# Optimization experiments

Hardware: AMD Instinct MI355X
Metric: run time of the kernel (lower is better)

Reference implementation:

```python
import jax, jax.numpy as jnp
import numpy as np

NH, K = 16, 4  # num_heads, num_points


def _ln(x, g, b):
    m = x.mean(-1, keepdims=True)
    v = jnp.var(x, axis=-1, keepdims=True)
    return (x - m) / jnp.sqrt(v + 1e-5) * g + b


def setup_inputs() -> dict:
    key = jax.random.key(0)
    ks = jax.random.split(key, 12)
    B, S, D = 16, 1024, 1024
    HD = D // NH
    def lin(k, fi, fo, scale=1.0):
        return jax.random.normal(k, (fi, fo), jnp.float32) * (scale / np.sqrt(fi))
    z = lambda n: jnp.zeros((n,), jnp.float32)
    return {
        "source": jax.random.normal(ks[0], (B, S, D), jnp.float32),
        "target": jax.random.normal(ks[1], (B, S, D), jnp.float32),
        "Wq": lin(ks[2], D, D), "bq": z(D),
        "Wo1": lin(ks[3], HD, 64), "bo1": z(64),
        "Wo2": lin(ks[4], 64, 2 * K, 0.1), "bo2": z(2 * K),
        "Wa": lin(ks[5], HD, K), "ba": z(K),
        "Wv": lin(ks[6], D, D), "bv": z(D),
        "Wout": lin(ks[7], D, D), "bout": z(D),
        "gq": jnp.ones((D,), jnp.float32), "bq_ln": z(D),
        "gkv": jnp.ones((D,), jnp.float32), "bkv_ln": z(D),
        "gffn": jnp.ones((D,), jnp.float32), "bffn_ln": z(D),
        "W1": lin(ks[8], D, 4 * D), "b1": z(4 * D),
        "W2": lin(ks[9], 4 * D, D), "b2": z(D),
    }


def _forward(source, target, Wq, bq, Wo1, bo1, Wo2, bo2, Wa, ba, Wv, bv,
             Wout, bout, gq, bq_ln, gkv, bkv_ln, gffn, bffn_ln, W1, b1, W2, b2):
    B, S, D = source.shape
    HD = D // NH
    Hs = int(round(S ** 0.5)); Ws = Hs  # S = H*W square grid

    q_norm = _ln(source, gq, bq_ln)
    v_norm = _ln(target, gkv, bkv_ln)
    q = (q_norm @ Wq + bq).reshape(B, S, NH, HD)
    # value map per head: (B, NH, H, W, HD)
    v = (v_norm @ Wv + bv).reshape(B, Hs, Ws, NH, HD).transpose(0, 3, 1, 2, 4)
    v_flat = v.reshape(B, NH, Hs * Ws, HD)

    # learned offsets: tanh(MLP(q)) * 0.5, in normalized [-1,1] coords
    h = jax.nn.relu(q @ Wo1 + bo1)
    off = jnp.tanh((h @ Wo2 + bo2).reshape(B, S, NH, K, 2)) * 0.5

    # reference grid: ref_grid[i*W+j] = (ref_x[j], ref_y[i])
    rx = jnp.linspace(-1.0, 1.0, Ws)
    ry = jnp.linspace(-1.0, 1.0, Hs)
    gx, gy = jnp.meshgrid(rx, ry)  # 'xy' indexing
    ref = jnp.stack([gx, gy], -1).reshape(S, 2)
    pts = ref[None, :, None, None, :] + off  # (B, S, NH, K, 2), last dim = (x, y)

    # grid_sample, bilinear, align_corners=True, padding_mode='zeros'
    x = (pts[..., 0] + 1.0) * 0.5 * (Ws - 1)
    y = (pts[..., 1] + 1.0) * 0.5 * (Hs - 1)
    x = jnp.moveaxis(x, 1, 2)  # (B, NH, S, K)
    y = jnp.moveaxis(y, 1, 2)
    x0 = jnp.floor(x); y0 = jnp.floor(y)
    wx1 = x - x0; wy1 = y - y0
    x0i = x0.astype(jnp.int32); y0i = y0.astype(jnp.int32)

    def gather(xi, yi, w):
        m = (xi >= 0) & (xi <= Ws - 1) & (yi >= 0) & (yi <= Hs - 1)
        idx = jnp.clip(yi, 0, Hs - 1) * Ws + jnp.clip(xi, 0, Ws - 1)
        g = jnp.take_along_axis(v_flat, idx.reshape(B, NH, S * K, 1), axis=2)
        return g.reshape(B, NH, S, K, HD) * (w * m)[..., None]

    sampled = (gather(x0i, y0i, (1.0 - wx1) * (1.0 - wy1))
               + gather(x0i + 1, y0i, wx1 * (1.0 - wy1))
               + gather(x0i, y0i + 1, (1.0 - wx1) * wy1)
               + gather(x0i + 1, y0i + 1, wx1 * wy1))  # (B, NH, S, K, HD)

    attn = jax.nn.softmax(q @ Wa + ba, axis=-1)  # (B, S, NH, K)
    head_out = jnp.einsum('bsnk,bnskd->bsnd', attn, sampled).reshape(B, S, D)

    src = source + (head_out @ Wout + bout)
    f = jax.nn.gelu(_ln(src, gffn, bffn_ln) @ W1 + b1, approximate=False)
    return src + (f @ W2 + b2)


def reference(source, target, Wq, bq, Wo1, bo1, Wo2, bo2, Wa, ba, Wv, bv,
              Wout, bout, gq, bq_ln, gkv, bkv_ln, gffn, bffn_ln, W1, b1, W2, b2):
    return _forward(source, target, Wq, bq, Wo1, bo1, Wo2, bo2, Wa, ba, Wv, bv,
                    Wout, bout, gq, bq_ln, gkv, bkv_ln, gffn, bffn_ln, W1, b1, W2, b2)
```

## Files before the change

### kernel.cpp

```cpp
#include <hip/hip_runtime.h>

typedef __attribute__((ext_vector_type(8))) short short8;
typedef __attribute__((ext_vector_type(16))) float f32x16;

#define DEV __device__ __forceinline__

DEV float bf2f(unsigned short u) { return __uint_as_float(((unsigned)u) << 16); }
DEV unsigned short f2bf(float f) {
  unsigned u = __float_as_uint(f);
  u += 0x7FFF + ((u >> 16) & 1);
  return (unsigned short)(u >> 16);
}

#define GLOAD_LDS16(gptr, lptr)                                                              \
  __builtin_amdgcn_global_load_lds((const __attribute__((address_space(1))) void*)(gptr),   \
                                   (__attribute__((address_space(3))) void*)(lptr), 16, 0, 0)

__global__ __launch_bounds__(256) void wt_transpose_bf16(const float* __restrict__ W,
                                                         unsigned short* __restrict__ Wt,
                                                         int K, int N) {
  __shared__ float t[32][33];
  int k0 = blockIdx.x * 32, n0 = blockIdx.y * 32;
  int tx = threadIdx.x, ty = threadIdx.y;
#pragma unroll
  for (int i = 0; i < 4; ++i)
    t[ty + 8 * i][tx] = W[(long)(k0 + ty + 8 * i) * N + n0 + tx];
  __syncthreads();
#pragma unroll
  for (int i = 0; i < 4; ++i)
    Wt[(long)(n0 + ty + 8 * i) * K + k0 + tx] = f2bf(t[tx][ty + 8 * i]);
}

__global__ __launch_bounds__(256) void ln_to_bf16_dual(
    const float* __restrict__ x0, const float* __restrict__ g0, const float* __restrict__ b0,
    unsigned short* __restrict__ y0,
    const float* __restrict__ x1, const float* __restrict__ g1, const float* __restrict__ b1,
    unsigned short* __restrict__ y1) {
  const bool second = blockIdx.x >= 16384;
  const long row = second ? blockIdx.x - 16384 : blockIdx.x;
  const float* x = second ? x1 : x0;
  const float* g = second ? g1 : g0;
  const float* b = second ? b1 : b0;
  unsigned short* y = second ? y1 : y0;
  const int tid = threadIdx.x;
  float4 v = *(const float4*)(x + row * 1024 + tid * 4);
  float s = v.x + v.y + v.z + v.w;
  float s2 = v.x * v.x + v.y * v.y + v.z * v.z + v.w * v.w;
#pragma unroll
  for (int o = 32; o > 0; o >>= 1) { s += __shfl_down(s, o); s2 += __shfl_down(s2, o); }
  __shared__ float red[8];
  __shared__ float mv[2];
  int wv = tid >> 6, ln = tid & 63;
  if (ln == 0) { red[wv] = s; red[4 + wv] = s2; }
  __syncthreads();
  if (tid == 0) {
    float a = red[0] + red[1] + red[2] + red[3];
    float q = red[4] + red[5] + red[6] + red[7];
    float mean = a * (1.f / 1024.f);
    mv[0] = mean;
    mv[1] = rsqrtf(q * (1.f / 1024.f) - mean * mean + 1e-5f);
  }
  __syncthreads();
  float mean = mv[0], rstd = mv[1];
  float4 gg = *(const float4*)(g + tid * 4);
  float4 bb = *(const float4*)(b + tid * 4);
  ushort4 o;
  o.x = f2bf((v.x - mean) * rstd * gg.x + bb.x);
  o.y = f2bf((v.y - mean) * rstd * gg.y + bb.y);
  o.z = f2bf((v.z - mean) * rstd * gg.z + bb.z);
  o.w = f2bf((v.w - mean) * rstd * gg.w + bb.w);
  *(ushort4*)(y + row * 1024 + tid * 4) = o;
}

__global__ __launch_bounds__(256) void ln_to_bf16(const float* __restrict__ x,
                                                  const float* __restrict__ g,
                                                  const float* __restrict__ b,
                                                  unsigned short* __restrict__ y) {
  const long row = blockIdx.x;
  const int tid = threadIdx.x;
  float4 v = *(const float4*)(x + row * 1024 + tid * 4);
  float s = v.x + v.y + v.z + v.w;
  float s2 = v.x * v.x + v.y * v.y + v.z * v.z + v.w * v.w;
#pragma unroll
  for (int o = 32; o > 0; o >>= 1) { s += __shfl_down(s, o); s2 += __shfl_down(s2, o); }
  __shared__ float red[8];
  __shared__ float mv[2];
  int wv = tid >> 6, ln = tid & 63;
  if (ln == 0) { red[wv] = s; red[4 + wv] = s2; }
  __syncthreads();
  if (tid == 0) {
    float a = red[0] + red[1] + red[2] + red[3];
    float q = red[4] + red[5] + red[6] + red[7];
    float mean = a * (1.f / 1024.f);
    mv[0] = mean;
    mv[1] = rsqrtf(q * (1.f / 1024.f) - mean * mean + 1e-5f);
  }
  __syncthreads();
  float mean = mv[0], rstd = mv[1];
  float4 gg = *(const float4*)(g + tid * 4);
  float4 bb = *(const float4*)(b + tid * 4);
  ushort4 o;
  o.x = f2bf((v.x - mean) * rstd * gg.x + bb.x);
  o.y = f2bf((v.y - mean) * rstd * gg.y + bb.y);
  o.z = f2bf((v.z - mean) * rstd * gg.z + bb.z);
  o.w = f2bf((v.w - mean) * rstd * gg.w + bb.w);
  *(ushort4*)(y + row * 1024 + tid * 4) = o;
}

template <int EPI>
DEV void epi_store(void* out, const float* res, long grow, long gcol, int N, float val) {
  if (EPI == 0) {
    ((unsigned short*)out)[grow * N + gcol] = f2bf(val);
  } else if (EPI == 1) {
    const int b_ = (int)(grow >> 10), hw = (int)(grow & 1023);
    const int nh = (int)(gcol >> 6), hd = (int)(gcol & 63);
    ((unsigned short*)out)[((long)(b_ * 16 + nh) << 16) + hw * 64 + hd] = f2bf(val);
  } else if (EPI == 2) {
    ((float*)out)[grow * N + gcol] = val + res[grow * N + gcol];
  } else if (EPI == 3) {
    const float c = 0.79788456080286536f;
    float t = tanhf(c * (val + 0.044715f * val * val * val));
    ((unsigned short*)out)[grow * N + gcol] = f2bf(0.5f * val * (1.f + t));
  } else {
    ((float*)out)[grow * N + gcol] = val + res[grow * N + gcol];
  }
}

template <int EPI>
__global__ __launch_bounds__(256, 4) void gemm32(const unsigned short* __restrict__ A,
                                                 const unsigned short* __restrict__ Bt,
                                                 const float* __restrict__ bias,
                                                 const float* __restrict__ res,
                                                 void* __restrict__ out,
                                                 int N, int K, int ldb, int n_mt) {
  __shared__ __align__(16) char smem[32768];
  const int tid = threadIdx.x;
  const int wave = tid >> 6, lane = tid & 63;
  const int wm = wave >> 1, wn = wave & 1;

  const int st = blockIdx.x >> 5, wi = blockIdx.x & 31;
  const int nsm = n_mt >> 3;
  const int stm = st % nsm, stn = st / nsm;
  const long row0 = (long)(stm * 8 + (wi & 7)) * 128;
  const long col0 = (long)(stn * 4 + (wi >> 3)) * 128;

  f32x16 acc[2][2];
#pragma unroll
  for (int i = 0; i < 2; ++i)
#pragma unroll
    for (int n = 0; n < 2; ++n)
#pragma unroll
      for (int r = 0; r < 16; ++r) acc[i][n][r] = 0.f;

  const int rin = lane >> 3, ch = lane & 7;

  for (int kt = 0; kt < K; kt += 64) {
#pragma unroll
    for (int i = 0; i < 4; ++i) {
      const int c = wave * 4 + i;
      const int r = c * 8 + rin;
      const int kg = ch ^ ((r >> 1) & 7);
      GLOAD_LDS16(A + (row0 + r) * (long)K + kt + kg * 8, smem + c * 1024);
      GLOAD_LDS16(Bt + (col0 + r) * (long)ldb + kt + kg * 8, smem + 16384 + c * 1024);
    }
    asm volatile("s_waitcnt vmcnt(0)" ::: "memory");
    __syncthreads();
#pragma unroll
    for (int ks = 0; ks < 4; ++ks) {
      short8 af[2], bfr[2];
      const int kc = ks * 2 + (lane >> 5);
#pragma unroll
      for (int mi = 0; mi < 2; ++mi) {
        const int rowa = wm * 64 + mi * 32 + (lane & 31);
        af[mi] = *(const short8*)(smem + rowa * 128 + (kc ^ ((rowa >> 1) & 7)) * 16);
      }
#pragma unroll
      for (int ni = 0; ni < 2; ++ni) {
        const int rowb = wn * 64 + ni * 32 + (lane & 31);
        bfr[ni] = *(const short8*)(smem + 16384 + rowb * 128 + (kc ^ ((rowb >> 1) & 7)) * 16);
      }
#pragma unroll
      for (int mi = 0; mi < 2; ++mi)
#pragma unroll
        for (int ni = 0; ni < 2; ++ni)
          acc[mi][ni] =
              __builtin_amdgcn_mfma_f32_32x32x16_bf16(af[mi], bfr[ni], acc[mi][ni], 0, 0, 0);
    }
    __syncthreads();
  }

  const int lc = lane & 31, lh = lane >> 5;
#pragma unroll
  for (int mi = 0; mi < 2; ++mi)
#pragma unroll
    for (int ni = 0; ni < 2; ++ni) {
      const long gcol = col0 + wn * 64 + ni * 32 + lc;
      const float bvv = (EPI == 5) ? 0.f : bias[gcol];
#pragma unroll
      for (int reg = 0; reg < 16; ++reg) {
        const long grow = row0 + wm * 64 + mi * 32 + (reg & 3) + 8 * (reg >> 2) + 4 * lh;
        epi_store<EPI>(out, res, grow, gcol, N, acc[mi][ni][reg] + bvv);
      }
    }
}

__global__ __launch_bounds__(256) void offset_attn_mlp(
    const unsigned short* __restrict__ qf,
    const float* __restrict__ Wo1, const float* __restrict__ bo1,
    const float* __restrict__ Wo2, const float* __restrict__ bo2,
    const float* __restrict__ Wa, const float* __restrict__ ba,
    float* __restrict__ coords) {
  const int r = blockIdx.x * 256 + threadIdx.x;
  const int s = (r >> 4) & 1023;

  float qr[64];
  const unsigned short* qp = qf + (long)r * 64;
#pragma unroll
  for (int i = 0; i < 8; ++i) {
    short8 v = *(const short8*)(qp + 8 * i);
#pragma unroll
    for (int j = 0; j < 8; ++j) qr[8 * i + j] = bf2f((unsigned short)v[j]);
  }

  float off[8];
#pragma unroll
  for (int o = 0; o < 8; ++o) off[o] = bo2[o];

#pragma unroll 1
  for (int jj = 0; jj < 8; ++jj) {
    float hacc[8];
#pragma unroll
    for (int o = 0; o < 8; ++o) hacc[o] = bo1[jj * 8 + o];
#pragma unroll
    for (int i = 0; i < 64; ++i) {
      const float qv = qr[i];
#pragma unroll
      for (int o = 0; o < 8; ++o) hacc[o] = fmaf(qv, Wo1[i * 64 + jj * 8 + o], hacc[o]);
    }
#pragma unroll
    for (int jo = 0; jo < 8; ++jo) {
      const float hj = fmaxf(hacc[jo], 0.f);
      const int j = jj * 8 + jo;
#pragma unroll
      for (int o = 0; o < 8; ++o) off[o] = fmaf(hj, Wo2[j * 8 + o], off[o]);
    }
  }

  float lg[4];
#pragma unroll
  for (int k = 0; k < 4; ++k) lg[k] = ba[k];
#pragma unroll
  for (int i = 0; i < 64; ++i) {
    const float qv = qr[i];
#pragma unroll
    for (int k = 0; k < 4; ++k) lg[k] = fmaf(qv, Wa[i * 4 + k], lg[k]);
  }
  const float mx = fmaxf(fmaxf(lg[0], lg[1]), fmaxf(lg[2], lg[3]));
  const float e0 = expf(lg[0] - mx), e1 = expf(lg[1] - mx), e2 = expf(lg[2] - mx),
              e3 = expf(lg[3] - mx);
  const float inv = 1.f / (e0 + e1 + e2 + e3);

  const float sx = (float)(s & 31), sy = (float)(s >> 5);
  float4 xv, yv, av;
  xv.x = sx + tanhf(off[0]) * 7.75f; yv.x = sy + tanhf(off[1]) * 7.75f;
  xv.y = sx + tanhf(off[2]) * 7.75f; yv.y = sy + tanhf(off[3]) * 7.75f;
  xv.z = sx + tanhf(off[4]) * 7.75f; yv.z = sy + tanhf(off[5]) * 7.75f;
  xv.w = sx + tanhf(off[6]) * 7.75f; yv.w = sy + tanhf(off[7]) * 7.75f;
  av.x = e0 * inv; av.y = e1 * inv; av.z = e2 * inv; av.w = e3 * inv;
  float* cp = coords + (long)r * 16;
  *(float4*)(cp + 0) = xv;
  *(float4*)(cp + 4) = yv;
  *(float4*)(cp + 8) = av;
}

__global__ __launch_bounds__(256) void deform_gather(
    const unsigned short* __restrict__ v_flat, const float* __restrict__ coords,
    unsigned short* __restrict__ head_out) {
  const int tid = threadIdx.x, wave = tid >> 6, lane = tid & 63;
  const int m = blockIdx.x * 4 + wave;
  const int b = m >> 14, nh = (m >> 10) & 15, s = m & 1023;
  const long r = (long)(b * 1024 + s) * 16 + nh;

  float cf = 0.f;
  if (lane < 12) cf = coords[r * 16 + lane];
  const unsigned short* vb = v_flat + ((long)(b * 16 + nh) << 16);

  float o = 0.f;
#pragma unroll
  for (int k = 0; k < 4; ++k) {
    const float xp = __shfl(cf, k), yp = __shfl(cf, 4 + k), ak = __shfl(cf, 8 + k);
    const float x0f = floorf(xp), y0f = floorf(yp);
    const int x0 = (int)x0f, y0 = (int)y0f;
    const float wx1 = xp - x0f, wy1 = yp - y0f;
    const float wx0 = 1.f - wx1, wy0 = 1.f - wy1;
    float smp = 0.f;
#pragma unroll
    for (int cn = 0; cn < 4; ++cn) {
      const int xi = x0 + (cn & 1), yi = y0 + (cn >> 1);
      const float w = (cn & 1 ? wx1 : wx0) * (cn >> 1 ? wy1 : wy0);
      const bool msk = (xi >= 0) & (xi <= 31) & (yi >= 0) & (yi <= 31);
      const int xc = min(max(xi, 0), 31), yc = min(max(yi, 0), 31);
      const float vv = bf2f(vb[(yc * 32 + xc) * 64 + lane]);
      smp = fmaf(vv, msk ? w : 0.f, smp);
    }
    o = fmaf(ak, smp, o);
  }
  head_out[r * 64 + lane] = f2bf(o);
}

extern "C" void kernel_launch(void* const* d_in, const int* in_sizes, int n_in,
                              void* d_out, int out_size, void* d_ws, size_t ws_size,
                              hipStream_t stream) {
  const float* source = (const float*)d_in[0];
  const float* target = (const float*)d_in[1];
  const float* Wq = (const float*)d_in[2];
  const float* bq = (const float*)d_in[3];
  const float* Wo1 = (const float*)d_in[4];
  const float* bo1 = (const float*)d_in[5];
  const float* Wo2 = (const float*)d_in[6];
  const float* bo2 = (const float*)d_in[7];
  const float* Wa = (const float*)d_in[8];
  const float* ba = (const float*)d_in[9];
  const float* Wv = (const float*)d_in[10];
  const float* bv = (const float*)d_in[11];
  const float* Wout = (const float*)d_in[12];
  const float* bout = (const float*)d_in[13];
  const float* gq = (const float*)d_in[14];
  const float* bq_ln = (const float*)d_in[15];
  const float* gkv = (const float*)d_in[16];
  const float* bkv_ln = (const float*)d_in[17];
  const float* gffn = (const float*)d_in[18];
  const float* bffn_ln = (const float*)d_in[19];
  const float* W1 = (const float*)d_in[20];
  const float* b1 = (const float*)d_in[21];
  const float* W2 = (const float*)d_in[22];
  const float* b2 = (const float*)d_in[23];

  char* ws = (char*)d_ws;
  const size_t MB = 1u << 20;
  if (ws_size < 150 * MB) return;
  const bool big = (ws_size >= 182 * MB);

  unsigned short* q_norm = (unsigned short*)(ws + 0);
  unsigned short* v_flat = (unsigned short*)(ws + 0);
  unsigned short* v_norm = (unsigned short*)(ws + 32 * MB);
  float* coords = (float*)(ws + 32 * MB);
  unsigned short* qf = (unsigned short*)(ws + 64 * MB);
  unsigned short* head_out = (unsigned short*)(ws + 96 * MB);
  unsigned short* ffn_in = (unsigned short*)(big ? ws + 128 * MB : ws + 32 * MB);
  unsigned short* f_buf = (unsigned short*)(big ? ws + 0 : ws + 64 * MB);
  char* wbase = big ? ws + 160 * MB : ws + 128 * MB;
  unsigned short* Wq_t = (unsigned short*)(wbase + 0);
  unsigned short* Wv_t = (unsigned short*)(wbase + 2 * MB);
  unsigned short* Wout_t = (unsigned short*)(wbase + 4 * MB);
  unsigned short* W1_t = (unsigned short*)(wbase + 6 * MB);
  unsigned short* W2_t = (unsigned short*)(wbase + 14 * MB);
  float* src = (float*)d_out;

  dim3 tb(32, 8);
  wt_transpose_bf16<<<dim3(32, 32), tb, 0, stream>>>(Wq, Wq_t, 1024, 1024);
  wt_transpose_bf16<<<dim3(32, 32), tb, 0, stream>>>(Wv, Wv_t, 1024, 1024);
  wt_transpose_bf16<<<dim3(32, 32), tb, 0, stream>>>(Wout, Wout_t, 1024, 1024);
  wt_transpose_bf16<<<dim3(32, 128), tb, 0, stream>>>(W1, W1_t, 1024, 4096);
  wt_transpose_bf16<<<dim3(128, 32), tb, 0, stream>>>(W2, W2_t, 4096, 1024);

  ln_to_bf16_dual<<<32768, 256, 0, stream>>>(source, gq, bq_ln, q_norm,
                                             target, gkv, bkv_ln, v_norm);

  gemm32<0><<<1024, 256, 0, stream>>>(q_norm, Wq_t, bq, nullptr, qf, 1024, 1024, 1024, 128);
  gemm32<1><<<1024, 256, 0, stream>>>(v_norm, Wv_t, bv, nullptr, v_flat, 1024, 1024, 1024, 128);

  offset_attn_mlp<<<1024, 256, 0, stream>>>(qf, Wo1, bo1, Wo2, bo2, Wa, ba, coords);
  deform_gather<<<65536, 256, 0, stream>>>(v_flat, coords, head_out);

  gemm32<2><<<1024, 256, 0, stream>>>(head_out, Wout_t, bout, source, src, 1024, 1024, 1024, 128);

  ln_to_bf16<<<16384, 256, 0, stream>>>(src, gffn, bffn_ln, ffn_in);

  if (big) {
    gemm32<3><<<4096, 256, 0, stream>>>(ffn_in, W1_t, b1, nullptr, f_buf, 4096, 1024, 1024, 128);
    gemm32<2><<<1024, 256, 0, stream>>>(f_buf, W2_t, b2, src, src, 1024, 4096, 4096, 128);
  } else {
    gemm32<3><<<2048, 256, 0, stream>>>(ffn_in, W1_t, b1, nullptr, f_buf, 2048, 1024, 1024, 128);
    gemm32<2><<<1024, 256, 0, stream>>>(f_buf, W2_t, b2, src, src, 1024, 2048, 4096, 128);
    gemm32<3><<<2048, 256, 0, stream>>>(ffn_in, W1_t + (long)2048 * 1024, b1 + 2048,
                                        nullptr, f_buf, 2048, 1024, 1024, 128);
    gemm32<5><<<1024, 256, 0, stream>>>(f_buf, W2_t + 2048, nullptr, src, src, 1024, 2048, 4096, 128);
  }
}
```

Measured before the change: 702.2 us.

## Use warp-specialized producer/consumer GEMM for the FFN up-projection

Adds a gemm_pc kernel with 512 threads per block. Four producer waves issue global-to-LDS loads into a double buffer while four consumer waves run MFMA on the other buffer. It replaces gemm32 for the W1 GEMM on the big path only. The aim is to overlap memory loads with compute. The cost is twice the threads per block, 64KB of LDS, and a block-wide barrier every k-tile, which may lower occupancy.

New measurement: 742.3 us. 5.7% more time.

```diff
diff --git a/kernel.cpp b/kernel.cpp
--- a/kernel.cpp
+++ b/kernel.cpp
@@ -202,6 +202,102 @@
         epi_store<EPI>(out, res, grow, gcol, N, acc[mi][ni][reg] + bvv);
       }
     }
+}
+
+template <int EPI>
+__global__ __launch_bounds__(512, 4) void gemm_pc(const unsigned short* __restrict__ A,
+                                                  const unsigned short* __restrict__ Bt,
+                                                  const float* __restrict__ bias,
+                                                  const float* __restrict__ res,
+                                                  void* __restrict__ out,
+                                                  int N, int K, int ldb, int n_mt) {
+  __shared__ __align__(16) char smem[65536];
+  const int tid = threadIdx.x;
+  const int wave = tid >> 6, lane = tid & 63;
+  const bool producer = wave >= 4;
+
+  const int st = blockIdx.x >> 5, wi = blockIdx.x & 31;
+  const int nsm = n_mt >> 3;
+  const long row0 = (long)((st % nsm) * 8 + (wi & 7)) * 128;
+  const long col0 = (long)((st / nsm) * 4 + (wi >> 3)) * 128;
+  const int NT = K >> 6;
+
+  f32x16 acc[2][2];
+#pragma unroll
+  for (int i = 0; i < 2; ++i)
+#pragma unroll
+    for (int n = 0; n < 2; ++n)
+#pragma unroll
+      for (int r = 0; r < 16; ++r) acc[i][n][r] = 0.f;
+
+  const int wm = wave >> 1, wn = wave & 1;
+  const int p = wave & 3;
+  const int rin = lane >> 3, ch = lane & 7;
+
+  auto STAGE = [&](int buf, int kt) {
+#pragma unroll
+    for (int i = 0; i < 4; ++i) {
+      const int c = p * 4 + i;
+      const int r = c * 8 + rin;
+      const int kg = ch ^ ((r >> 1) & 7);
+      GLOAD_LDS16(A + (row0 + r) * (long)K + kt + kg * 8, smem + buf * 32768 + c * 1024);
+      GLOAD_LDS16(Bt + (col0 + r) * (long)ldb + kt + kg * 8,
+                  smem + buf * 32768 + 16384 + c * 1024);
+    }
+  };
+
+  if (producer) {
+    STAGE(0, 0);
+    asm volatile("s_waitcnt vmcnt(0)" ::: "memory");
+  }
+  __syncthreads();
+
+  for (int t = 0; t < NT; ++t) {
+    if (!producer) {
+      const char* sm = smem + (t & 1) * 32768;
+#pragma unroll
+      for (int ks = 0; ks < 4; ++ks) {
+        short8 af[2], bfr[2];
+        const int kc = ks * 2 + (lane >> 5);
+#pragma unroll
+        for (int mi = 0; mi < 2; ++mi) {
+          const int rowa = wm * 64 + mi * 32 + (lane & 31);
+          af[mi] = *(const short8*)(sm + rowa * 128 + (kc ^ ((rowa >> 1) & 7)) * 16);
+        }
+#pragma unroll
+        for (int ni = 0; ni < 2; ++ni) {
+          const int rowb = wn * 64 + ni * 32 + (lane & 31);
+          bfr[ni] = *(const short8*)(sm + 16384 + rowb * 128 + (kc ^ ((rowb >> 1) & 7)) * 16);
+        }
+#pragma unroll
+        for (int mi = 0; mi < 2; ++mi)
+#pragma unroll
+          for (int ni = 0; ni < 2; ++ni)
+            acc[mi][ni] =
+                __builtin_amdgcn_mfma_f32_32x32x16_bf16(af[mi], bfr[ni], acc[mi][ni], 0, 0, 0);
+      }
+    } else {
+      if (t + 1 < NT) STAGE((t + 1) & 1, (t + 1) << 6);
+      asm volatile("s_waitcnt vmcnt(0)" ::: "memory");
+    }
+    __syncthreads();
+  }
+
+  if (!producer) {
+    const int lc = lane & 31, lh = lane >> 5;
+#pragma unroll
+    for (int mi = 0; mi < 2; ++mi)
+#pragma unroll
+      for (int ni = 0; ni < 2; ++ni) {
+        const long gcol = col0 + wn * 64 + ni * 32 + lc;
+        const float bvv = (EPI == 5) ? 0.f : bias[gcol];
+#pragma unroll
+        for (int reg = 0; reg < 16; ++reg) {
+          const long grow = row0 + wm * 64 + mi * 32 + (reg & 3) + 8 * (reg >> 2) + 4 * lh;
+          epi_store<EPI>(out, res, grow, gcol, N, acc[mi][ni][reg] + bvv);
+        }
+      }
+  }
 }
 
 __global__ __launch_bounds__(256) void offset_attn_mlp(
@@ -378,7 +474,7 @@
   ln_to_bf16<<<16384, 256, 0, stream>>>(src, gffn, bffn_ln, ffn_in);
 
   if (big) {
-    gemm32<3><<<4096, 256, 0, stream>>>(ffn_in, W1_t, b1, nullptr, f_buf, 4096, 1024, 1024, 128);
+    gemm_pc<3><<<4096, 512, 0, stream>>>(ffn_in, W1_t, b1, nullptr, f_buf, 4096, 1024, 1024, 128);
     gemm32<2><<<1024, 256, 0, stream>>>(f_buf, W2_t, b2, src, src, 1024, 4096, 4096, 128);
   } else {
     gemm32<3><<<2048, 256, 0, stream>>>(ffn_in, W1_t, b1, nullptr, f_buf, 2048, 1024, 1024, 128);
```
